# Kernel tuning notes

Hardware: AMD Instinct MI355X
Metric: run time of the kernel (lower is better)

Reference implementation:

```python
import jax, jax.numpy as jnp
import numpy as np

V, D, DI, S, B, NI = 32000, 1024, 768, 512, 8, 197
EPS = 1e-5

def _ln(x, g, b):
    m = jnp.mean(x, axis=-1, keepdims=True)
    v = jnp.var(x, axis=-1, keepdims=True)
    return (x - m) * jax.lax.rsqrt(v + EPS) * g + b

def _pos_enc(seq_len, d):
    pos = np.arange(seq_len)[:, None].astype(np.float32)
    i = np.arange(0, d, 2).astype(np.float32)
    ang = pos / np.power(10000.0, i / d)
    pe = np.zeros((seq_len, d), dtype=np.float32)
    pe[:, 0::2] = np.sin(ang)
    pe[:, 1::2] = np.cos(ang)
    return jnp.asarray(pe)

def setup_inputs() -> dict:
    key = jax.random.key(0)
    ks = jax.random.split(key, 24)
    def rn(k, shape, scale=0.02):
        return jax.random.normal(k, shape, dtype=jnp.float32) * scale
    return {
        'tokens': jax.random.randint(ks[0], (B, S), 0, V),
        'img_emb': jax.random.normal(ks[1], (B, NI, DI), dtype=jnp.float32),
        'emb_table': rn(ks[2], (V, D), 1.0),
        'Wq1': rn(ks[3], (D, D)), 'bq1': jnp.zeros((D,), jnp.float32),
        'Wk1': rn(ks[4], (D, D)), 'bk1': jnp.zeros((D,), jnp.float32),
        'Wv1': rn(ks[5], (D, D)), 'bv1': jnp.zeros((D,), jnp.float32),
        'g1': jnp.ones((D,), jnp.float32), 'b1': jnp.zeros((D,), jnp.float32),
        'Wq2': rn(ks[6], (D, D)), 'bq2': jnp.zeros((D,), jnp.float32),
        'Wk2': rn(ks[7], (DI, D)), 'bk2': jnp.zeros((D,), jnp.float32),
        'Wv2': rn(ks[8], (DI, D)), 'bv2': jnp.zeros((D,), jnp.float32),
        'g2': jnp.ones((D,), jnp.float32), 'b2': jnp.zeros((D,), jnp.float32),
        'Wp': rn(ks[9], (D, V)), 'bp': jnp.zeros((V,), jnp.float32),
    }

def _forward(tokens, img_emb, emb_table, Wq1, bq1, Wk1, bk1, Wv1, bv1, g1, b1,
             Wq2, bq2, Wk2, bk2, Wv2, bv2, g2, b2, Wp, bp):
    scale = 1.0 / jnp.sqrt(jnp.float32(D))
    x = emb_table[tokens] + _pos_enc(S, D)[None]  # [B,S,D]
    # masked (causal) self-attention
    Q = x @ Wq1 + bq1
    K = x @ Wk1 + bk1
    Vv = x @ Wv1 + bv1
    attn = jnp.einsum('bqd,bkd->bqk', Q, K) * scale
    causal = jnp.tril(jnp.ones((S, S), dtype=bool))
    attn = jnp.where(causal[None], attn, -jnp.inf)
    A = jax.nn.softmax(attn, axis=-1)
    x = _ln(A @ Vv + x, g1, b1)
    # cross-attention over image tokens
    Q2 = x @ Wq2 + bq2
    K2 = img_emb @ Wk2 + bk2
    V2 = img_emb @ Wv2 + bv2
    A2 = jax.nn.softmax(jnp.einsum('bqd,bkd->bqk', Q2, K2) * scale, axis=-1)
    x = _ln(A2 @ V2 + x, g2, b2)
    # vocab projection (note: Decoder.forward never calls self.ff)
    return x @ Wp + bp  # [B,S,V]

def reference(tokens, img_emb, emb_table, Wq1, bq1, Wk1, bk1, Wv1, bv1, g1, b1,
              Wq2, bq2, Wk2, bk2, Wv2, bv2, g2, b2, Wp, bp):
    return _forward(tokens, img_emb, emb_table, Wq1, bq1, Wk1, bk1, Wv1, bv1, g1, b1,
                    Wq2, bq2, Wk2, bk2, Wv2, bv2, g2, b2, Wp, bp)
```

## Files before the change

### kernel.cpp

```cpp
#include <hip/hip_runtime.h>
#include <hip/hip_bf16.h>


#define DEV __device__ __forceinline__

typedef __bf16 bf16x8 __attribute__((ext_vector_type(8)));
typedef float f32x4 __attribute__((ext_vector_type(4)));
typedef unsigned int u32;
typedef __hip_bfloat16 bf16;

DEV void llds16(const void* g, void* l) {
  __builtin_amdgcn_global_load_lds((const __attribute__((address_space(1))) u32*)g,
                                   (__attribute__((address_space(3))) u32*)l, 16, 0, 0);
}

DEV float wredsum(float v){
#pragma unroll
  for (int o = 32; o; o >>= 1) v += __shfl_xor(v, o, 64);
  return v;
}
DEV float wredmax(float v){
#pragma unroll
  for (int o = 32; o; o >>= 1) v = fmaxf(v, __shfl_xor(v, o, 64));
  return v;
}

DEV void store_out(float* p, float v){ *p = v; }
DEV void store_out(bf16* p, float v){ *p = __float2bfloat16(v); }

__global__ __launch_bounds__(512, 1) void gemm256_kernel(
    const bf16* __restrict__ A, const bf16* __restrict__ Bt, float* __restrict__ C,
    const float* __restrict__ bias, int M, int N, int K, int lda, int ldb, int ldc)
{
  __shared__ alignas(16) char lds[131072];
  const int tid  = threadIdx.x;
  const int wave = tid >> 6, lane = tid & 63;
  const int lo = lane & 15, hi = lane >> 4;
  const int hi2 = hi ^ ((lo >> 1) & 3);
  const int wr = wave >> 2, wc = wave & 3;
  const int koff = (((lane & 3) ^ ((lane >> 3) & 3)) << 3);

  const int nbx = M >> 8, nby = N >> 8;
  const int nwg = nbx * nby;
  int id = blockIdx.x;
  int g = (nwg & 7) ? id : ((id & 7) * (nwg >> 3) + (id >> 3));
  const int row0 = (g % nbx) * 256;
  const int col0 = (g / nbx) * 256;
  const int srow = lane >> 2;
  const int NT = K >> 5;

  auto stageA = [&](int t) {
    char* base = lds + (t & 3) * 32768;
    const int kk = (t << 5) + koff;
#pragma unroll
    for (int j = 0; j < 2; j++) {
      const int r = (j * 8 + wave) * 16 + srow;
      llds16(A + (long)(row0 + r) * lda + kk, base + (j * 8 + wave) * 1024);
    }
  };
  auto stageB = [&](int t) {
    char* base = lds + (t & 3) * 32768 + 16384;
    const int kk = (t << 5) + koff;
#pragma unroll
    for (int j = 0; j < 2; j++) {
      const int r = (j * 8 + wave) * 16 + srow;
      llds16(Bt + (long)(col0 + r) * ldb + kk, base + (j * 8 + wave) * 1024);
    }
  };

  stageA(0); stageB(0);
  stageA(1); stageB(1);
  stageA(2); stageB(2);
  asm volatile("s_waitcnt vmcnt(8)" ::: "memory");
  __builtin_amdgcn_s_barrier();
  asm volatile("" ::: "memory");

  f32x4 acc[8][4] = {};

  for (int t = 0; t < NT; t++) {
    char* As = lds + (t & 3) * 32768;
    char* Bs = As + 16384;
    bf16x8 af[4], bfv[4];
#pragma unroll
    for (int m = 0; m < 4; m++)
      af[m] = *(const bf16x8*)(As + ((wr * 128 + m * 16 + lo) << 6) + (hi2 << 4));
#pragma unroll
    for (int n = 0; n < 4; n++)
      bfv[n] = *(const bf16x8*)(Bs + ((wc * 64 + n * 16 + lo) << 6) + (hi2 << 4));
    if (t + 3 < NT) stageA(t + 3);
    __builtin_amdgcn_s_setprio(1);
#pragma unroll
    for (int m = 0; m < 4; m++)
#pragma unroll
      for (int n = 0; n < 4; n++)
        acc[m][n] = __builtin_amdgcn_mfma_f32_16x16x32_bf16(af[m], bfv[n], acc[m][n], 0, 0, 0);
    __builtin_amdgcn_s_setprio(0);
    asm volatile("" ::: "memory");
    __builtin_amdgcn_s_barrier();
    asm volatile("" ::: "memory");
#pragma unroll
    for (int m = 0; m < 4; m++)
      af[m] = *(const bf16x8*)(As + ((wr * 128 + (m + 4) * 16 + lo) << 6) + (hi2 << 4));
    if (t + 3 < NT) stageB(t + 3);
    __builtin_amdgcn_s_setprio(1);
#pragma unroll
    for (int m = 0; m < 4; m++)
#pragma unroll
      for (int n = 0; n < 4; n++)
        acc[m + 4][n] = __builtin_amdgcn_mfma_f32_16x16x32_bf16(af[m], bfv[n], acc[m + 4][n], 0, 0, 0);
    __builtin_amdgcn_s_setprio(0);
    if (t < NT - 3)       asm volatile("s_waitcnt vmcnt(8)" ::: "memory");
    else if (t == NT - 3) asm volatile("s_waitcnt vmcnt(4)" ::: "memory");
    else                  asm volatile("s_waitcnt vmcnt(0)" ::: "memory");
    __builtin_amdgcn_s_barrier();
    asm volatile("" ::: "memory");
  }

#pragma unroll
  for (int m = 0; m < 8; m++) {
    const int r = row0 + wr * 128 + m * 16 + hi * 4;
#pragma unroll
    for (int n = 0; n < 4; n++) {
      const int c = col0 + wc * 64 + n * 16 + lo;
      const float bb = bias ? bias[c] : 0.0f;
#pragma unroll
      for (int j = 0; j < 4; j++)
        C[(long)(r + j) * ldc + c] = acc[m][n][j] + bb;
    }
  }
}

template<typename OutT>
__global__ __launch_bounds__(256) void gemm_bt_kernel(
    const bf16* __restrict__ A, const bf16* __restrict__ Bt, OutT* __restrict__ C,
    const float* __restrict__ bias, int M, int N, int K,
    int lda, int ldb, int ldc, long sA, long sB, long sC)
{
  A  += (long)blockIdx.z * sA;
  Bt += (long)blockIdx.z * sB;
  C  += (long)blockIdx.z * sC;
  __shared__ alignas(16) bf16 As[128*32];
  __shared__ alignas(16) bf16 Bs[128*32];
  const int tid = threadIdx.x;
  const int wave = tid >> 6, lane = tid & 63;
  const int lo = lane & 15, hi = lane >> 4;
  const int hi2 = hi ^ ((lo >> 1) & 3);
  const int wr = wave >> 1, wc = wave & 1;
  const int row0 = blockIdx.x * 128, col0 = blockIdx.y * 128;
  const int srow  = lane >> 2;
  const int skoff = (((lane & 3) ^ ((lane >> 3) & 3)) << 3);

  f32x4 acc[4][4] = {};

  for (int k0 = 0; k0 < K; k0 += 32) {
#pragma unroll
    for (int c = 0; c < 2; ++c) {
      const int seg = c*4 + wave;
      int ra = row0 + seg*16 + srow; ra = ra < M ? ra : M-1;
      llds16(A + (long)ra*lda + (k0 + skoff), (char*)As + seg*1024);
      int rb = col0 + seg*16 + srow; rb = rb < N ? rb : N-1;
      llds16(Bt + (long)rb*ldb + (k0 + skoff), (char*)Bs + seg*1024);
    }
    __syncthreads();
    bf16x8 af[4], bfv[4];
#pragma unroll
    for (int m = 0; m < 4; m++)
      af[m] = *(const bf16x8*)((const char*)As + (wr*64 + m*16 + lo)*64 + hi2*16);
#pragma unroll
    for (int n = 0; n < 4; n++)
      bfv[n] = *(const bf16x8*)((const char*)Bs + (wc*64 + n*16 + lo)*64 + hi2*16);
#pragma unroll
    for (int m = 0; m < 4; m++)
#pragma unroll
      for (int n = 0; n < 4; n++)
        acc[m][n] = __builtin_amdgcn_mfma_f32_16x16x32_bf16(af[m], bfv[n], acc[m][n], 0, 0, 0);
    __syncthreads();
  }

#pragma unroll
  for (int m = 0; m < 4; m++) {
    const int rbase = row0 + wr*64 + m*16 + hi*4;
#pragma unroll
    for (int n = 0; n < 4; n++) {
      const int cc = col0 + wc*64 + n*16 + lo;
      if (cc >= N) continue;
      const float bb = bias ? bias[cc] : 0.0f;
#pragma unroll
      for (int j = 0; j < 4; j++) {
        const int rr = rbase + j;
        if (rr < M) store_out(&C[(long)rr*ldc + cc], acc[m][n][j] + bb);
      }
    }
  }
}

__global__ __launch_bounds__(256) void wprep_kernel(
    const float* __restrict__ W, bf16* __restrict__ Wt, int K, int N)
{
  __shared__ bf16 t[32][33];
  const int k0 = blockIdx.x * 32, n0 = blockIdx.y * 32;
  const int tx = threadIdx.x & 31, ty = threadIdx.x >> 5;
#pragma unroll
  for (int i = 0; i < 4; i++)
    t[ty + i*8][tx] = __float2bfloat16(W[(long)(k0 + ty + i*8)*N + n0 + tx]);
  __syncthreads();
#pragma unroll
  for (int i = 0; i < 4; i++)
    Wt[(long)(n0 + ty + i*8)*K + k0 + tx] = t[tx][ty + i*8];
}

__global__ __launch_bounds__(256) void transpose_pad_kernel(
    const bf16* __restrict__ in, bf16* __restrict__ out,
    int R, int Cc, int outLD, long inBatch, long outBatch)
{
  in  += (long)blockIdx.z * inBatch;
  out += (long)blockIdx.z * outBatch;
  __shared__ bf16 t[32][33];
  const int r0 = blockIdx.x * 32, c0 = blockIdx.y * 32;
  const int tx = threadIdx.x & 31, ty = threadIdx.x >> 5;
#pragma unroll
  for (int i = 0; i < 4; i++) {
    const int r = r0 + ty + i*8;
    bf16 v = __float2bfloat16(0.0f);
    if (r < R) v = in[(long)r*Cc + c0 + tx];
    t[ty + i*8][tx] = v;
  }
  __syncthreads();
#pragma unroll
  for (int i = 0; i < 4; i++) {
    const int oc = r0 + tx;
    const int orow = c0 + ty + i*8;
    if (oc < outLD) out[(long)orow*outLD + oc] = t[tx][ty + i*8];
  }
}

__global__ __launch_bounds__(256) void embed_kernel(
    const int* __restrict__ tok, const float* __restrict__ tbl,
    float* __restrict__ xf, bf16* __restrict__ xb)
{
  const int row = blockIdx.x;
  const int s = row & 511;
  const float pos = (float)s;
  const float* te = tbl + (long)tok[row] * 1024;
  const int d0 = threadIdx.x * 4;
  float4 v = *(const float4*)(te + d0);
  float o[4] = {v.x, v.y, v.z, v.w};
#pragma unroll
  for (int k = 0; k < 4; k++) {
    const int d = d0 + k;
    const int i2 = d & ~1;
    const float ang = pos * powf(10000.0f, -(float)i2 * (1.0f/1024.0f));
    o[k] += (d & 1) ? cosf(ang) : sinf(ang);
  }
  *(float4*)(xf + (long)row*1024 + d0) = make_float4(o[0], o[1], o[2], o[3]);
#pragma unroll
  for (int k = 0; k < 4; k++) xb[(long)row*1024 + d0 + k] = __float2bfloat16(o[k]);
}

__global__ __launch_bounds__(256) void cvt_bf16_kernel(const float* __restrict__ in, bf16* __restrict__ out, long n)
{
  long i = (long)blockIdx.x * blockDim.x + threadIdx.x;
  if (i < n) out[i] = __float2bfloat16(in[i]);
}

__global__ __launch_bounds__(64) void softmax_causal_kernel(
    const float* __restrict__ Sc, bf16* __restrict__ P)
{
  const int row = blockIdx.x;
  const int q = row & 511;
  const float* srow = Sc + (long)row * 512;
  bf16* prow = P + (long)row * 512;
  const int lane = threadIdx.x;
  const float scale = 0.03125f;
  float mx = -1e30f;
  for (int j = lane; j <= q; j += 64) mx = fmaxf(mx, srow[j]);
  mx = wredmax(mx);
  float sum = 0.0f;
  for (int j = lane; j <= q; j += 64) sum += expf((srow[j] - mx) * scale);
  sum = wredsum(sum);
  const float inv = 1.0f / sum;
  for (int j = lane; j < 512; j += 64) {
    float p = (j <= q) ? expf((srow[j] - mx) * scale) * inv : 0.0f;
    prow[j] = __float2bfloat16(p);
  }
}

__global__ __launch_bounds__(64) void softmax_cross_kernel(
    const float* __restrict__ Sc, bf16* __restrict__ P)
{
  const int row = blockIdx.x;
  const float* srow = Sc + (long)row * 224;
  bf16* prow = P + (long)row * 224;
  const int lane = threadIdx.x;
  const float scale = 0.03125f;
  float mx = -1e30f;
  for (int j = lane; j < 197; j += 64) mx = fmaxf(mx, srow[j]);
  mx = wredmax(mx);
  float sum = 0.0f;
  for (int j = lane; j < 197; j += 64) sum += expf((srow[j] - mx) * scale);
  sum = wredsum(sum);
  const float inv = 1.0f / sum;
  for (int j = lane; j < 224; j += 64) {
    float p = (j < 197) ? expf((srow[j] - mx) * scale) * inv : 0.0f;
    prow[j] = __float2bfloat16(p);
  }
}

__global__ __launch_bounds__(256) void add_ln_kernel(
    const float* __restrict__ Acc, const float* __restrict__ Res,
    const float* __restrict__ g, const float* __restrict__ b,
    float* __restrict__ outf, bf16* __restrict__ outb)
{
  const int row = blockIdx.x;
  const float* a = Acc + (long)row * 1024;
  const float* r = Res + (long)row * 1024;
  float vals[4], s = 0.0f, ss = 0.0f;
#pragma unroll
  for (int i = 0; i < 4; i++) {
    const int d = threadIdx.x + i*256;
    const float v = a[d] + r[d];
    vals[i] = v; s += v; ss += v*v;
  }
  s = wredsum(s); ss = wredsum(ss);
  __shared__ float sh[8];
  const int wave = threadIdx.x >> 6, lane = threadIdx.x & 63;
  if (lane == 0) { sh[wave] = s; sh[wave+4] = ss; }
  __syncthreads();
  s  = sh[0] + sh[1] + sh[2] + sh[3];
  ss = sh[4] + sh[5] + sh[6] + sh[7];
  const float mean = s * (1.0f/1024.0f);
  const float var  = ss * (1.0f/1024.0f) - mean*mean;
  const float inv  = rsqrtf(var + 1e-5f);
#pragma unroll
  for (int i = 0; i < 4; i++) {
    const int d = threadIdx.x + i*256;
    const float y = (vals[i] - mean) * inv * g[d] + b[d];
    if (outf) outf[(long)row*1024 + d] = y;
    outb[(long)row*1024 + d] = __float2bfloat16(y);
  }
}

extern "C" void kernel_launch(void* const* d_in, const int* in_sizes, int n_in,
                              void* d_out, int out_size, void* d_ws, size_t ws_size,
                              hipStream_t stream) {
  const int*   tokens = (const int*)  d_in[0];
  const float* img    = (const float*)d_in[1];
  const float* emb    = (const float*)d_in[2];
  const float* Wq1    = (const float*)d_in[3];
  const float* bq1    = (const float*)d_in[4];
  const float* Wk1    = (const float*)d_in[5];
  const float* bk1    = (const float*)d_in[6];
  const float* Wv1    = (const float*)d_in[7];
  const float* bv1    = (const float*)d_in[8];
  const float* g1     = (const float*)d_in[9];
  const float* b1     = (const float*)d_in[10];
  const float* Wq2    = (const float*)d_in[11];
  const float* bq2    = (const float*)d_in[12];
  const float* Wk2    = (const float*)d_in[13];
  const float* bk2    = (const float*)d_in[14];
  const float* Wv2    = (const float*)d_in[15];
  const float* bv2    = (const float*)d_in[16];
  const float* g2     = (const float*)d_in[17];
  const float* b2     = (const float*)d_in[18];
  const float* Wp     = (const float*)d_in[19];
  const float* bp     = (const float*)d_in[20];
  float* out = (float*)d_out;

  const int B = 8, S = 512, D = 1024, DI = 768, NI = 197, NIP = 224, V = 32000;
  const int M = B * S;
  const int MI = B * NI;

  char* ws = (char*)d_ws;
  size_t off = 0;
  auto alloc = [&](size_t bytes) -> char* {
    char* p = ws + off; off += (bytes + 255) & ~(size_t)255; return p;
  };
  bf16* Wq1t = (bf16*)alloc((size_t)D*D*2);
  bf16* Wk1t = (bf16*)alloc((size_t)D*D*2);
  bf16* Wv1t = (bf16*)alloc((size_t)D*D*2);
  bf16* Wq2t = (bf16*)alloc((size_t)D*D*2);
  bf16* Wk2t = (bf16*)alloc((size_t)D*DI*2);
  bf16* Wv2t = (bf16*)alloc((size_t)D*DI*2);
  bf16* Wpt  = (bf16*)alloc((size_t)V*D*2);
  float* xf  = (float*)alloc((size_t)M*D*4);
  bf16*  xb  = (bf16*) alloc((size_t)M*D*2);
  bf16*  imgb= (bf16*) alloc((size_t)MI*DI*2);
  bf16*  Q   = (bf16*) alloc((size_t)M*D*2);
  bf16*  Kb  = (bf16*) alloc((size_t)M*D*2);
  bf16*  Vb  = (bf16*) alloc((size_t)M*D*2);
  bf16*  Vt  = (bf16*) alloc((size_t)M*D*2);
  float* sc1 = (float*)alloc((size_t)B*S*S*4);
  bf16*  P1  = (bf16*) alloc((size_t)B*S*S*2);
  float* ao1 = (float*)alloc((size_t)M*D*4);
  float* x2f = (float*)alloc((size_t)M*D*4);
  bf16*  x2b = (bf16*) alloc((size_t)M*D*2);
  bf16*  Q2  = (bf16*) alloc((size_t)M*D*2);
  bf16*  K2  = (bf16*) alloc((size_t)MI*D*2);
  bf16*  V2  = (bf16*) alloc((size_t)MI*D*2);
  bf16*  V2t = (bf16*) alloc((size_t)B*D*NIP*2);
  float* sc2 = (float*)alloc((size_t)B*S*NIP*4);
  bf16*  P2  = (bf16*) alloc((size_t)B*S*NIP*2);
  float* ao2 = (float*)alloc((size_t)M*D*4);
  bf16*  x3b = (bf16*) alloc((size_t)M*D*2);
  (void)ws_size; (void)in_sizes; (void)n_in; (void)out_size;

  wprep_kernel<<<dim3(D/32,  D/32), 256, 0, stream>>>(Wq1, Wq1t, D, D);
  wprep_kernel<<<dim3(D/32,  D/32), 256, 0, stream>>>(Wk1, Wk1t, D, D);
  wprep_kernel<<<dim3(D/32,  D/32), 256, 0, stream>>>(Wv1, Wv1t, D, D);
  wprep_kernel<<<dim3(D/32,  D/32), 256, 0, stream>>>(Wq2, Wq2t, D, D);
  wprep_kernel<<<dim3(DI/32, D/32), 256, 0, stream>>>(Wk2, Wk2t, DI, D);
  wprep_kernel<<<dim3(DI/32, D/32), 256, 0, stream>>>(Wv2, Wv2t, DI, D);
  wprep_kernel<<<dim3(D/32,  V/32), 256, 0, stream>>>(Wp,  Wpt,  D, V);

  embed_kernel<<<M, 256, 0, stream>>>(tokens, emb, xf, xb);
  {
    long n = (long)MI * DI;
    cvt_bf16_kernel<<<(int)((n + 255)/256), 256, 0, stream>>>(img, imgb, n);
  }

  auto gemmF = [&](const bf16* A, const bf16* Bt, float* C, const float* bias,
                   int m, int n, int k, int lda, int ldb, int ldc,
                   long sA, long sB, long sC, int batch) {
    dim3 g((m+127)/128, (n+127)/128, batch);
    gemm_bt_kernel<float><<<g, 256, 0, stream>>>(A, Bt, C, bias, m, n, k, lda, ldb, ldc, sA, sB, sC);
  };
  auto gemmB = [&](const bf16* A, const bf16* Bt, bf16* C, const float* bias,
                   int m, int n, int k, int lda, int ldb, int ldc,
                   long sA, long sB, long sC, int batch) {
    dim3 g((m+127)/128, (n+127)/128, batch);
    gemm_bt_kernel<bf16><<<g, 256, 0, stream>>>(A, Bt, C, bias, m, n, k, lda, ldb, ldc, sA, sB, sC);
  };

  gemmB(xb, Wq1t, Q,  bq1, M, D, D, D, D, D, 0, 0, 0, 1);
  gemmB(xb, Wk1t, Kb, bk1, M, D, D, D, D, D, 0, 0, 0, 1);
  gemmB(xb, Wv1t, Vb, bv1, M, D, D, D, D, D, 0, 0, 0, 1);
  transpose_pad_kernel<<<dim3(S/32, D/32, B), 256, 0, stream>>>(
      Vb, Vt, S, D, S, (long)S*D, (long)D*S);
  gemmF(Q, Kb, sc1, nullptr, S, S, D, D, D, S, (long)S*D, (long)S*D, (long)S*S, B);
  softmax_causal_kernel<<<M, 64, 0, stream>>>(sc1, P1);
  gemmF(P1, Vt, ao1, nullptr, S, D, S, S, S, D, (long)S*S, (long)D*S, (long)S*D, B);
  add_ln_kernel<<<M, 256, 0, stream>>>(ao1, xf, g1, b1, x2f, x2b);

  gemmB(x2b, Wq2t, Q2, bq2, M, D, D, D, D, D, 0, 0, 0, 1);
  gemmB(imgb, Wk2t, K2, bk2, MI, D, DI, DI, DI, D, 0, 0, 0, 1);
  gemmB(imgb, Wv2t, V2, bv2, MI, D, DI, DI, DI, D, 0, 0, 0, 1);
  transpose_pad_kernel<<<dim3((NIP+31)/32, D/32, B), 256, 0, stream>>>(
      V2, V2t, NI, D, NIP, (long)NI*D, (long)D*NIP);
  gemmF(Q2, K2, sc2, nullptr, S, NI, D, D, D, NIP, (long)S*D, (long)NI*D, (long)S*NIP, B);
  softmax_cross_kernel<<<M, 64, 0, stream>>>(sc2, P2);
  gemmF(P2, V2t, ao2, nullptr, S, D, NIP, NIP, NIP, D, (long)S*NIP, (long)D*NIP, (long)S*D, B);
  add_ln_kernel<<<M, 256, 0, stream>>>(ao2, x2f, g2, b2, nullptr, x3b);

  {
    dim3 g((M/256) * (V/256));
    gemm256_kernel<<<g, 512, 0, stream>>>(x3b, Wpt, out, bp, M, V, D, D, D, V);
  }
}
```

Measured before the change: 792.5 us.

## Restructure 256x256 GEMM main loop into double-buffered 64-wide K steps

The big bf16 GEMM moves from a 4-stage ring of 32-wide K tiles to a 2-stage double buffer of 64-wide K tiles. Each tile is split into two K halves and two N halves, with a finer interleave of global-to-LDS prefetches, barriers and MFMA bursts. Fragments are loaded as 8 A rows and 2 B columns per sub-step, and sched_barrier pins the instruction order. The aim is to halve loop-iteration overhead and smooth LDS/MFMA overlap. In exchange there are more barriers per K step and less prefetch depth, so latency may be exposed.

Measured after the change: 805.9 us. Within noise of the previous version (+1.7%).

```diff
diff --git a/kernel.cpp b/kernel.cpp
--- a/kernel.cpp
+++ b/kernel.cpp
@@ -40,80 +40,84 @@
   const int wr = wave >> 2, wc = wave & 3;
   const int koff = (((lane & 3) ^ ((lane >> 3) & 3)) << 3);
 
-  const int nbx = M >> 8, nby = N >> 8;
-  const int nwg = nbx * nby;
+  const int nbx = M >> 8;
+  const int nwg = nbx * (N >> 8);
   int id = blockIdx.x;
   int g = (nwg & 7) ? id : ((id & 7) * (nwg >> 3) + (id >> 3));
   const int row0 = (g % nbx) * 256;
   const int col0 = (g / nbx) * 256;
+  const int NT = K >> 6;
   const int srow = lane >> 2;
-  const int NT = K >> 5;
-
-  auto stageA = [&](int t) {
-    char* base = lds + (t & 3) * 32768;
-    const int kk = (t << 5) + koff;
+
+  auto stageA = [&](int t, int ks) {
+    char* base = lds + ((t & 1) << 16) + (ks << 14);
+    const int kk = (t << 6) + (ks << 5) + koff;
 #pragma unroll
     for (int j = 0; j < 2; j++) {
-      const int r = (j * 8 + wave) * 16 + srow;
-      llds16(A + (long)(row0 + r) * lda + kk, base + (j * 8 + wave) * 1024);
+      const int seg = j * 8 + wave;
+      llds16(A + (long)(row0 + seg * 16 + srow) * lda + kk, base + seg * 1024);
     }
   };
-  auto stageB = [&](int t) {
-    char* base = lds + (t & 3) * 32768 + 16384;
-    const int kk = (t << 5) + koff;
+  auto stageB = [&](int t, int ks) {
+    char* base = lds + ((t & 1) << 16) + 32768 + (ks << 14);
+    const int kk = (t << 6) + (ks << 5) + koff;
 #pragma unroll
     for (int j = 0; j < 2; j++) {
-      const int r = (j * 8 + wave) * 16 + srow;
-      llds16(Bt + (long)(col0 + r) * ldb + kk, base + (j * 8 + wave) * 1024);
+      const int seg = j * 8 + wave;
+      llds16(Bt + (long)(col0 + seg * 16 + srow) * ldb + kk, base + seg * 1024);
     }
   };
 
-  stageA(0); stageB(0);
-  stageA(1); stageB(1);
-  stageA(2); stageB(2);
-  asm volatile("s_waitcnt vmcnt(8)" ::: "memory");
+  f32x4 acc[8][4] = {};
+  bf16x8 af[8], bfr[2];
+
+  stageA(0, 0); stageB(0, 0); stageA(0, 1); stageB(0, 1);
+  asm volatile("s_waitcnt vmcnt(4)" ::: "memory");
   __builtin_amdgcn_s_barrier();
-  asm volatile("" ::: "memory");
-
-  f32x4 acc[8][4] = {};
+  __builtin_amdgcn_sched_barrier(0);
 
   for (int t = 0; t < NT; t++) {
-    char* As = lds + (t & 3) * 32768;
-    char* Bs = As + 16384;
-    bf16x8 af[4], bfv[4];
-#pragma unroll
-    for (int m = 0; m < 4; m++)
-      af[m] = *(const bf16x8*)(As + ((wr * 128 + m * 16 + lo) << 6) + (hi2 << 4));
-#pragma unroll
-    for (int n = 0; n < 4; n++)
-      bfv[n] = *(const bf16x8*)(Bs + ((wc * 64 + n * 16 + lo) << 6) + (hi2 << 4));
-    if (t + 3 < NT) stageA(t + 3);
-    __builtin_amdgcn_s_setprio(1);
-#pragma unroll
-    for (int m = 0; m < 4; m++)
-#pragma unroll
-      for (int n = 0; n < 4; n++)
-        acc[m][n] = __builtin_amdgcn_mfma_f32_16x16x32_bf16(af[m], bfv[n], acc[m][n], 0, 0, 0);
-    __builtin_amdgcn_s_setprio(0);
-    asm volatile("" ::: "memory");
-    __builtin_amdgcn_s_barrier();
-    asm volatile("" ::: "memory");
-#pragma unroll
-    for (int m = 0; m < 4; m++)
-      af[m] = *(const bf16x8*)(As + ((wr * 128 + (m + 4) * 16 + lo) << 6) + (hi2 << 4));
-    if (t + 3 < NT) stageB(t + 3);
-    __builtin_amdgcn_s_setprio(1);
-#pragma unroll
-    for (int m = 0; m < 4; m++)
-#pragma unroll
-      for (int n = 0; n < 4; n++)
-        acc[m + 4][n] = __builtin_amdgcn_mfma_f32_16x16x32_bf16(af[m], bfv[n], acc[m + 4][n], 0, 0, 0);
-    __builtin_amdgcn_s_setprio(0);
-    if (t < NT - 3)       asm volatile("s_waitcnt vmcnt(8)" ::: "memory");
-    else if (t == NT - 3) asm volatile("s_waitcnt vmcnt(4)" ::: "memory");
-    else                  asm volatile("s_waitcnt vmcnt(0)" ::: "memory");
-    __builtin_amdgcn_s_barrier();
-    asm volatile("" ::: "memory");
+    char* sb = lds + ((t & 1) << 16);
+    const bool pre = (t + 1 < NT);
+#pragma unroll
+    for (int ks = 0; ks < 2; ks++) {
+#pragma unroll
+      for (int nh = 0; nh < 2; nh++) {
+        if (nh == 0) {
+#pragma unroll
+          for (int m = 0; m < 8; m++)
+            af[m] = *(const bf16x8*)(sb + (ks << 14) + ((wr * 128 + m * 16 + lo) << 6) + (hi2 << 4));
+        }
+#pragma unroll
+        for (int j = 0; j < 2; j++)
+          bfr[j] = *(const bf16x8*)(sb + 32768 + (ks << 14) + ((wc * 64 + (2 * nh + j) * 16 + lo) << 6) + (hi2 << 4));
+        if (pre) {
+          if (ks == 0 && nh == 0)      stageA(t + 1, 0);
+          else if (ks == 0)            stageB(t + 1, 0);
+          else if (nh == 0)            stageA(t + 1, 1);
+          else                         stageB(t + 1, 1);
+        }
+        __builtin_amdgcn_sched_barrier(0);
+        __builtin_amdgcn_s_barrier();
+        __builtin_amdgcn_sched_barrier(0);
+        __builtin_amdgcn_s_setprio(1);
+#pragma unroll
+        for (int m = 0; m < 8; m++)
+#pragma unroll
+          for (int j = 0; j < 2; j++)
+            acc[m][2 * nh + j] = __builtin_amdgcn_mfma_f32_16x16x32_bf16(af[m], bfr[j], acc[m][2 * nh + j], 0, 0, 0);
+        __builtin_amdgcn_s_setprio(0);
+        __builtin_amdgcn_sched_barrier(0);
+        if (ks == 0 && nh == 1) {
+          if (pre) asm volatile("s_waitcnt vmcnt(4)" ::: "memory");
+          else     asm volatile("s_waitcnt vmcnt(0)" ::: "memory");
+        } else if (ks == 1 && nh == 1 && pre) {
+          asm volatile("s_waitcnt vmcnt(4)" ::: "memory");
+        }
+        __builtin_amdgcn_s_barrier();
+        __builtin_amdgcn_sched_barrier(0);
+      }
+    }
   }
 
 #pragma unroll
```
